# Optimization experiments

Measured on AMD Instinct MI355X. Metric: run time of the kernel, lower is better.

The kernel has to match this reference:

```python
import jax, jax.numpy as jnp
import numpy as np

N_NODES = 50000
N_ENT = 100000
N_REL = 200
DE = 100
DR = 100
B = 16
E2 = 600000
U = 500


def setup_inputs() -> dict:
    key = jax.random.key(0)
    ks = jax.random.split(key, 16)
    f32 = jnp.float32
    return {
        "entity_table": jax.random.normal(ks[0], (N_ENT, DE), f32),
        "relation_table": jax.random.normal(ks[1], (N_REL, DR), f32),
        "total_unseen_embedding": jax.random.normal(ks[2], (U, DE), f32),
        "att_mu": jax.random.normal(ks[3], (2 * N_REL, B), f32) * 0.1,
        "basis_mu": jax.random.normal(ks[4], (B, DE + DR, DE), f32) * 0.05,
        "root_mu": jax.random.normal(ks[5], (DE, DE), f32) * 0.1,
        "bias_mu": jnp.zeros((DE,), f32),
        "att_sigma": jax.random.normal(ks[6], (2 * N_REL, B), f32) * 0.1,
        "basis_sigma": jax.random.normal(ks[7], (B, DE + DR, DE), f32) * 0.05,
        "root_sigma": jax.random.normal(ks[8], (DE, DE), f32) * 0.1,
        "bias_sigma": jnp.zeros((DE,), f32),
        "node_id": jax.random.randint(ks[9], (N_NODES,), 0, N_ENT),
        "edge_index": jax.random.randint(ks[10], (2, E2), 0, N_NODES),
        "edge_type": jax.random.randint(ks[11], (E2,), 0, 2 * N_REL),
        "rel_index": jax.random.randint(ks[12], (E2,), 0, N_REL),
        "unseen_index": jax.random.randint(ks[13], (U,), 0, N_NODES),
    }


def gen_conv(m, edge_type, dst, x, att, basis, root, bias, n_nodes):
    """Basis-decomposed relational conv with mean aggregation (GENConv).

    m: [E, in] per-edge concat(x_src, rel_emb); msg_e = m_e @ (att[type_e] @ basis).
    Computed as sum_b coeff[:, b] * (m @ basis[b]) to avoid an [E, in, out] gather.
    """
    coeff = att[edge_type]  # [E, B]
    msg = coeff[:, 0:1] * (m @ basis[0])
    for b in range(1, basis.shape[0]):
        msg = msg + coeff[:, b:b + 1] * (m @ basis[b])
    agg = jax.ops.segment_sum(msg, dst, num_segments=n_nodes)  # [N, out]
    cnt = jax.ops.segment_sum(jnp.ones((m.shape[0],), m.dtype), dst,
                              num_segments=n_nodes)
    agg = agg / jnp.maximum(cnt, 1.0)[:, None]  # scatter-mean, empty nodes -> 0
    return agg + x @ root + bias


def reference(entity_table, relation_table, total_unseen_embedding,
              att_mu, basis_mu, root_mu, bias_mu,
              att_sigma, basis_sigma, root_sigma, bias_sigma,
              node_id, edge_index, edge_type, rel_index, unseen_index):
    x = entity_table[node_id]  # [N, De]
    x = x.at[unseen_index].set(total_unseen_embedding)
    rel_emb = relation_table[rel_index]  # [E, Dr]
    src, dst = edge_index[0], edge_index[1]
    m = jnp.concatenate([x[src], rel_emb], axis=1)  # [E, De+Dr]
    n = x.shape[0]
    mu = gen_conv(m, edge_type, dst, x, att_mu, basis_mu, root_mu, bias_mu, n)
    logvar = gen_conv(m, edge_type, dst, x, att_sigma, basis_sigma,
                      root_sigma, bias_sigma, n)
    # eval mode: reparameterize -> mu, dropout -> identity
    unseen = mu[unseen_index]
    return unseen, mu[unseen_index], logvar[unseen_index]
```

## Files before the change

kernel.cpp:

```cpp
#include <hip/hip_runtime.h>
#include <stdint.h>

#define E2V     600000
#define NNODES  50000
#define UCNT    500
#define DE      100
#define DOUT    100
#define NB      16
#define KTOT    3328
#define KCH     104
#define MROWS   512
#define HASHN   2048
#define HCAP    64
#define NREG    586
#define ECAP    96
#define TRB     832
#define OUTN    (3*UCNT*DOUT)

using short8 = __attribute__((ext_vector_type(8))) short;
using f32x4  = __attribute__((ext_vector_type(4))) float;

static constexpr size_t align256(size_t x){ return (x + 255) & ~size_t(255); }
static constexpr size_t OFF_HCNT = 0;
static constexpr size_t OFF_IHEA = align256(OFF_HCNT + NREG*4);
static constexpr size_t OFF_INEX = OFF_IHEA + MROWS*4;
static constexpr size_t OFF_HBUF = align256(OFF_INEX + MROWS*4);
static constexpr size_t OFF_GM   = align256(OFF_HBUF + (size_t)NREG*HCAP*4);
static constexpr size_t OFF_GS   = OFF_GM + (size_t)MROWS*KTOT*2;
static constexpr size_t OFF_BTM  = align256(OFF_GS + (size_t)MROWS*KTOT*2);
static constexpr size_t OFF_BTS  = OFF_BTM + (size_t)DOUT*KTOT*2;

__device__ __forceinline__ unsigned short f2b(float f){
    uint32_t u = __float_as_uint(f);
    uint32_t r = (u + 0x7FFFu + ((u >> 16) & 1u)) >> 16;
    return (unsigned short)r;
}

__device__ __forceinline__ uint32_t hh(int key){
    return (((uint32_t)key * 2654435761u) >> 16) & (HASHN - 1);
}
__device__ __forceinline__ void hins(int* hk, int* hv, int key, int val){
    uint32_t idx = hh(key);
    while (true){
        int k = hk[idx];
        if (k == key){ atomicMax(&hv[idx], val); return; }
        if (k == -1){
            int old = atomicCAS(&hk[idx], -1, key);
            if (old == -1 || old == key){ atomicMax(&hv[idx], val); return; }
        }
        idx = (idx + 1) & (HASHN - 1);
    }
}
__device__ __forceinline__ int hlook(const int* hk, const int* hv, int key){
    uint32_t idx = hh(key);
    while (true){
        int k = hk[idx];
        if (k == key) return hv[idx];
        if (k == -1)  return -1;
        idx = (idx + 1) & (HASHN - 1);
    }
}

__device__ __forceinline__ float bt_src(const float* __restrict__ basis,
                                        const float* __restrict__ root,
                                        const float* __restrict__ bias,
                                        int k, int j){
    if (j >= 100) return 0.f;
    if (k < 3200) return basis[k*100 + j];
    if (k < 3300) return root[(k-3200)*100 + j];
    if (k == 3300) return bias[j];
    return 0.f;
}

__global__ __launch_bounds__(256) void k1(
        const int* __restrict__ unseen_index, const int* __restrict__ eidx,
        int* __restrict__ hcnt, uint32_t* __restrict__ hbuf,
        int* __restrict__ ihead, int* __restrict__ inext,
        const float* __restrict__ bm, const float* __restrict__ bs,
        const float* __restrict__ rm, const float* __restrict__ rs,
        const float* __restrict__ qm, const float* __restrict__ qs,
        unsigned short* __restrict__ btm, unsigned short* __restrict__ bts){
    __shared__ int hk[HASHN], hv[HASHN];
    __shared__ float tile[32][33];
    __shared__ uint32_t sHit[HCAP];
    __shared__ int sN, sIH[MROWS];
    int bx = blockIdx.x, tid = threadIdx.x;

    if (bx < NREG){
        for (int i = tid; i < HASHN; i += 256){ hk[i] = -1; hv[i] = -1; }
        if (tid == 0) sN = 0;
        __syncthreads();
        for (int u = tid; u < UCNT; u += 256) hins(hk, hv, unseen_index[u], u);
        __syncthreads();
        int e0 = bx*1024 + tid*4;
        if (e0 < E2V){
            int4 d = *(const int4*)(eidx + E2V + e0);
            int s;
            s = hlook(hk, hv, d.x); if (s >= 0){ int p = atomicAdd(&sN,1); if (p < HCAP) sHit[p] = ((uint32_t)s<<21)|(uint32_t)(e0);   }
            s = hlook(hk, hv, d.y); if (s >= 0){ int p = atomicAdd(&sN,1); if (p < HCAP) sHit[p] = ((uint32_t)s<<21)|(uint32_t)(e0+1); }
            s = hlook(hk, hv, d.z); if (s >= 0){ int p = atomicAdd(&sN,1); if (p < HCAP) sHit[p] = ((uint32_t)s<<21)|(uint32_t)(e0+2); }
            s = hlook(hk, hv, d.w); if (s >= 0){ int p = atomicAdd(&sN,1); if (p < HCAP) sHit[p] = ((uint32_t)s<<21)|(uint32_t)(e0+3); }
        }
        __syncthreads();
        int n = sN < HCAP ? sN : HCAP;
        if (tid == 0) hcnt[bx] = n;
        if (tid < n) hbuf[bx*HCAP + tid] = sHit[tid];
        return;
    }
    if (bx < NREG + TRB){
        int b2 = bx - NREG;
        int kt = b2 % KCH, jt = (b2 / KCH) & 3, br = b2 / (KCH*4);
        const float* basis = br ? bs : bm;
        const float* root  = br ? rs : rm;
        const float* bias  = br ? qs : qm;
        unsigned short* bt = br ? bts : btm;
        int k0 = kt*32, j0 = jt*32;
        int tx = tid & 31, ty = tid >> 5;
        for (int r = ty; r < 32; r += 8)
            tile[r][tx] = bt_src(basis, root, bias, k0 + r, j0 + tx);
        __syncthreads();
        for (int r = ty; r < 32; r += 8){
            int j = j0 + r;
            if (j < 100) bt[(size_t)j*KTOT + k0 + tx] = f2b(tile[tx][r]);
        }
        return;
    }
    for (int i = tid; i < HASHN; i += 256){ hk[i] = -1; hv[i] = -1; }
    for (int i = tid; i < MROWS; i += 256) sIH[i] = -1;
    __syncthreads();
    for (int u = tid; u < UCNT; u += 256) hins(hk, hv, unseen_index[u], u);
    __syncthreads();
    for (int u = tid; u < UCNT; u += 256){
        int slot = hlook(hk, hv, unseen_index[u]);
        inext[u] = atomicExch(&sIH[slot], u);
    }
    __syncthreads();
    for (int i = tid; i < MROWS; i += 256) ihead[i] = sIH[i];
}

__global__ __launch_bounds__(256) void k_g(
        const int* __restrict__ hcnt, const uint32_t* __restrict__ hbuf,
        const int* __restrict__ unseen_index,
        const int* __restrict__ eidx,
        const int* __restrict__ etype, const int* __restrict__ rel_index,
        const int* __restrict__ node_id,
        const float* __restrict__ ent, const float* __restrict__ unseen,
        const float* __restrict__ rel,
        const float* __restrict__ am, const float* __restrict__ as_,
        unsigned short* __restrict__ Gm, unsigned short* __restrict__ Gs,
        float* __restrict__ out){
    int slot = blockIdx.x;
    int tid  = threadIdx.x;
    {
        int z0 = slot * 294;
        for (int i = z0 + tid; i < z0 + 294 && i < OUTN; i += 256) out[i] = 0.f;
    }
    __shared__ int hk[HASHN], hv[HASHN];
    __shared__ int sEdge[ECAP], sNE;
    __shared__ __align__(16) float sM[8][200];
    __shared__ __align__(16) float sAm[8][16], sAs[8][16];
    __shared__ const float* sPX[8];
    __shared__ const float* sPR[8];
    __shared__ int sT[8];

    for (int i = tid; i < HASHN; i += 256){ hk[i] = -1; hv[i] = -1; }
    if (tid == 0) sNE = 0;
    __syncthreads();
    for (int u = tid; u < UCNT; u += 256) hins(hk, hv, unseen_index[u], u);
    __syncthreads();
    for (int r = tid; r < NREG; r += 256){
        int c = hcnt[r];
        for (int i = 0; i < c; ++i){
            uint32_t h = hbuf[r*HCAP + i];
            if ((int)(h >> 21) == slot){
                int p = atomicAdd(&sNE, 1);
                if (p < ECAP) sEdge[p] = (int)(h & 0x1FFFFFu);
            }
        }
    }
    __syncthreads();
    int nT = sNE;
    int nE = nT > ECAP ? ECAP : nT;

    float gm[16], gs[16];
    #pragma unroll
    for (int b = 0; b < NB; ++b){ gm[b] = 0.f; gs[b] = 0.f; }

    for (int c0 = 0; c0 < nE; c0 += 8){
        int kc = nE - c0; if (kc > 8) kc = 8;
        if (tid < kc){
            int e = sEdge[c0 + tid];
            sT[tid] = etype[e];
            int s = eidx[e];
            int p = hlook(hk, hv, s);
            sPX[tid] = (p >= 0) ? unseen + (size_t)p*DE : ent + (size_t)node_id[s]*DE;
            sPR[tid] = rel + (size_t)rel_index[e]*DE;
        }
        __syncthreads();
        for (int q = tid; q < kc*50; q += 256){
            int eL = q / 50, s = q % 50;
            const float* base = (s < 25) ? sPX[eL] : sPR[eL];
            int off = (s < 25) ? s*4 : (s-25)*4;
            float4 v = *(const float4*)(base + off);
            int kb = (s < 25) ? s*4 : (s-25)*4 + 100;
            *(float4*)&sM[eL][kb] = v;
        }
        if (tid < kc*16){
            int eL = tid >> 4, b = tid & 15;
            int t = sT[eL];
            sAm[eL][b] = am[t*NB + b];
            sAs[eL][b] = as_[t*NB + b];
        }
        __syncthreads();
        if (tid < 200){
            for (int e = 0; e < kc; ++e){
                float mk = sM[e][tid];
                const float4* pa = (const float4*)&sAm[e][0];
                const float4* ps = (const float4*)&sAs[e][0];
                #pragma unroll
                for (int q = 0; q < 4; ++q){
                    float4 va = pa[q], vs = ps[q];
                    gm[q*4+0] += va.x*mk; gm[q*4+1] += va.y*mk;
                    gm[q*4+2] += va.z*mk; gm[q*4+3] += va.w*mk;
                    gs[q*4+0] += vs.x*mk; gs[q*4+1] += vs.y*mk;
                    gs[q*4+2] += vs.z*mk; gs[q*4+3] += vs.w*mk;
                }
            }
        }
        __syncthreads();
    }
    size_t row = (size_t)slot * KTOT;
    float inv = 1.f / fmaxf((float)nT, 1.f);
    if (tid < 200){
        #pragma unroll
        for (int b = 0; b < NB; ++b){
            Gm[row + b*200 + tid] = f2b(gm[b] * inv);
            Gs[row + b*200 + tid] = f2b(gs[b] * inv);
        }
    }
    if (tid < 100){
        float xv = (slot < UCNT) ? unseen[(size_t)slot*DE + tid] : 0.f;
        unsigned short h = f2b(xv);
        Gm[row + 3200 + tid] = h; Gs[row + 3200 + tid] = h;
    } else if (tid == 100){
        Gm[row + 3300] = f2b(1.f); Gs[row + 3300] = f2b(1.f);
    } else if (tid > 100 && tid < 128){
        Gm[row + 3200 + tid] = 0; Gs[row + 3200 + tid] = 0;
    }
}

__global__ __launch_bounds__(448) void k_gemm(
        const unsigned short* __restrict__ Gm, const unsigned short* __restrict__ Gs,
        const unsigned short* __restrict__ Btm, const unsigned short* __restrict__ Bts,
        const int* __restrict__ ihead, const int* __restrict__ inext,
        float* __restrict__ out){
    int bid = blockIdx.x;
    int br  = bid >> 7;
    int m32 = (bid >> 3) & 15;
    int ks  = bid & 7;
    int jt  = threadIdx.x >> 6;
    int lane = threadIdx.x & 63;
    const unsigned short* A  = br ? Gs : Gm;
    const unsigned short* Bt = br ? Bts : Btm;
    int rowa = lane & 15, ko = (lane >> 4) * 8;
    int j0 = (jt == 6) ? 84 : jt*16;
    int col = j0 + rowa;
    size_t kbase = (size_t)ks*416 + ko;
    const unsigned short* bp  = Bt + (size_t)col*KTOT + kbase;
    const unsigned short* ap0 = A  + (size_t)(m32*32 + rowa)*KTOT + kbase;
    const unsigned short* ap1 = ap0 + (size_t)16*KTOT;
    f32x4 acc0 = {0.f,0.f,0.f,0.f}, acc1 = {0.f,0.f,0.f,0.f};
    #pragma unroll
    for (int kc = 0; kc < 13; ++kc){
        short8 bv = *(const short8*)(bp + kc*32);
        acc0 = __builtin_amdgcn_mfma_f32_16x16x32_bf16(*(const short8*)(ap0 + kc*32), bv, acc0, 0, 0, 0);
        acc1 = __builtin_amdgcn_mfma_f32_16x16x32_bf16(*(const short8*)(ap1 + kc*32), bv, acc1, 0, 0, 0);
    }
    if (jt < 6 || col >= 96){
        #pragma unroll
        for (int mi = 0; mi < 2; ++mi){
            f32x4 acc = mi ? acc1 : acc0;
            int r0 = m32*32 + mi*16 + (lane >> 4)*4;
            #pragma unroll
            for (int r = 0; r < 4; ++r){
                int u = ihead[r0 + r];
                while (u >= 0){
                    if (br == 0){
                        atomicAdd(&out[(size_t)u*100 + col], acc[r]);
                        atomicAdd(&out[(size_t)(UCNT + u)*100 + col], acc[r]);
                    } else {
                        atomicAdd(&out[(size_t)(2*UCNT + u)*100 + col], acc[r]);
                    }
                    u = inext[u];
                }
            }
        }
    }
}

extern "C" void kernel_launch(void* const* d_in, const int* in_sizes, int n_in,
                              void* d_out, int out_size, void* d_ws, size_t ws_size,
                              hipStream_t stream){
    const float* ent        = (const float*)d_in[0];
    const float* rel_table  = (const float*)d_in[1];
    const float* unseen_emb = (const float*)d_in[2];
    const float* att_mu     = (const float*)d_in[3];
    const float* basis_mu   = (const float*)d_in[4];
    const float* root_mu    = (const float*)d_in[5];
    const float* bias_mu    = (const float*)d_in[6];
    const float* att_sig    = (const float*)d_in[7];
    const float* basis_sig  = (const float*)d_in[8];
    const float* root_sig   = (const float*)d_in[9];
    const float* bias_sig   = (const float*)d_in[10];
    const int* node_id      = (const int*)d_in[11];
    const int* edge_index   = (const int*)d_in[12];
    const int* edge_type    = (const int*)d_in[13];
    const int* rel_index    = (const int*)d_in[14];
    const int* unseen_index = (const int*)d_in[15];
    float* out = (float*)d_out;
    char* ws = (char*)d_ws;

    int* hcnt       = (int*)(ws + OFF_HCNT);
    int* ihead      = (int*)(ws + OFF_IHEA);
    int* inext      = (int*)(ws + OFF_INEX);
    uint32_t* hbuf  = (uint32_t*)(ws + OFF_HBUF);
    unsigned short* Gm  = (unsigned short*)(ws + OFF_GM);
    unsigned short* Gs  = (unsigned short*)(ws + OFF_GS);
    unsigned short* Btm = (unsigned short*)(ws + OFF_BTM);
    unsigned short* Bts = (unsigned short*)(ws + OFF_BTS);

    k1<<<NREG + TRB + 1, 256, 0, stream>>>(unseen_index, edge_index,
        hcnt, hbuf, ihead, inext,
        basis_mu, basis_sig, root_mu, root_sig, bias_mu, bias_sig, Btm, Bts);
    k_g<<<MROWS, 256, 0, stream>>>(hcnt, hbuf, unseen_index, edge_index, edge_type,
        rel_index, node_id, ent, unseen_emb, rel_table, att_mu, att_sig, Gm, Gs, out);
    k_gemm<<<256, 448, 0, stream>>>(Gm, Gs, Btm, Bts, ihead, inext, out);
}
```

Baseline: 53.21 us.

## Bucket edges per slot via global atomics and replace atomic output with split-K reduce kernel

The edge filter now uses fewer blocks, each scanning 8192 edges. Hits are appended directly into per-slot global edge lists with atomic counters, and each hit also stores a precomputed source slot. This removes the per-block hash rebuild and the full hit-buffer scan in k_g. The GEMM now uses 13 K-splits, writes partials to a buffer instead of atomically adding into the output, and a new k_out kernel sums the partials and scatters them to duplicate unseen indices. The cost is an extra memset and an extra kernel launch, plus global atomic contention on the slot counters.

```diff
diff --git a/kernel.cpp b/kernel.cpp
--- a/kernel.cpp
+++ b/kernel.cpp
@@ -8,27 +8,27 @@
 #define DOUT    100
 #define NB      16
 #define KTOT    3328
-#define KCH     104
 #define MROWS   512
 #define HASHN   2048
-#define HCAP    64
-#define NREG    586
-#define ECAP    96
+#define CAP     96
+#define NF      74
 #define TRB     832
-#define OUTN    (3*UCNT*DOUT)
+#define NKS     13
 
 using short8 = __attribute__((ext_vector_type(8))) short;
 using f32x4  = __attribute__((ext_vector_type(4))) float;
 
 static constexpr size_t align256(size_t x){ return (x + 255) & ~size_t(255); }
-static constexpr size_t OFF_HCNT = 0;
-static constexpr size_t OFF_IHEA = align256(OFF_HCNT + NREG*4);
+static constexpr size_t OFF_SCNT = 0;
+static constexpr size_t OFF_IHEA = align256(OFF_SCNT + MROWS*4);
 static constexpr size_t OFF_INEX = OFF_IHEA + MROWS*4;
-static constexpr size_t OFF_HBUF = align256(OFF_INEX + MROWS*4);
-static constexpr size_t OFF_GM   = align256(OFF_HBUF + (size_t)NREG*HCAP*4);
+static constexpr size_t OFF_ELIS = align256(OFF_INEX + MROWS*4);
+static constexpr size_t OFF_ESRC = align256(OFF_ELIS + (size_t)MROWS*CAP*4);
+static constexpr size_t OFF_GM   = align256(OFF_ESRC + (size_t)MROWS*CAP*2);
 static constexpr size_t OFF_GS   = OFF_GM + (size_t)MROWS*KTOT*2;
 static constexpr size_t OFF_BTM  = align256(OFF_GS + (size_t)MROWS*KTOT*2);
 static constexpr size_t OFF_BTS  = OFF_BTM + (size_t)DOUT*KTOT*2;
+static constexpr size_t OFF_P    = align256(OFF_BTS + (size_t)DOUT*KTOT*2);
 
 __device__ __forceinline__ unsigned short f2b(float f){
     uint32_t u = __float_as_uint(f);
@@ -74,7 +74,7 @@
 
 __global__ __launch_bounds__(256) void k1(
         const int* __restrict__ unseen_index, const int* __restrict__ eidx,
-        int* __restrict__ hcnt, uint32_t* __restrict__ hbuf,
+        int* __restrict__ scnt, int* __restrict__ elist, short* __restrict__ esrc,
         int* __restrict__ ihead, int* __restrict__ inext,
         const float* __restrict__ bm, const float* __restrict__ bs,
         const float* __restrict__ rm, const float* __restrict__ rs,
@@ -82,34 +82,38 @@
         unsigned short* __restrict__ btm, unsigned short* __restrict__ bts){
     __shared__ int hk[HASHN], hv[HASHN];
     __shared__ float tile[32][33];
-    __shared__ uint32_t sHit[HCAP];
-    __shared__ int sN, sIH[MROWS];
+    __shared__ int sIH[MROWS];
     int bx = blockIdx.x, tid = threadIdx.x;
 
-    if (bx < NREG){
+    if (bx < NF){
         for (int i = tid; i < HASHN; i += 256){ hk[i] = -1; hv[i] = -1; }
-        if (tid == 0) sN = 0;
         __syncthreads();
         for (int u = tid; u < UCNT; u += 256) hins(hk, hv, unseen_index[u], u);
         __syncthreads();
-        int e0 = bx*1024 + tid*4;
-        if (e0 < E2V){
+        for (int r = 0; r < 8; ++r){
+            int e0 = bx*8192 + (r*256 + tid)*4;
+            if (e0 >= E2V) break;
             int4 d = *(const int4*)(eidx + E2V + e0);
-            int s;
-            s = hlook(hk, hv, d.x); if (s >= 0){ int p = atomicAdd(&sN,1); if (p < HCAP) sHit[p] = ((uint32_t)s<<21)|(uint32_t)(e0);   }
-            s = hlook(hk, hv, d.y); if (s >= 0){ int p = atomicAdd(&sN,1); if (p < HCAP) sHit[p] = ((uint32_t)s<<21)|(uint32_t)(e0+1); }
-            s = hlook(hk, hv, d.z); if (s >= 0){ int p = atomicAdd(&sN,1); if (p < HCAP) sHit[p] = ((uint32_t)s<<21)|(uint32_t)(e0+2); }
-            s = hlook(hk, hv, d.w); if (s >= 0){ int p = atomicAdd(&sN,1); if (p < HCAP) sHit[p] = ((uint32_t)s<<21)|(uint32_t)(e0+3); }
-        }
-        __syncthreads();
-        int n = sN < HCAP ? sN : HCAP;
-        if (tid == 0) hcnt[bx] = n;
-        if (tid < n) hbuf[bx*HCAP + tid] = sHit[tid];
+            #pragma unroll
+            for (int j = 0; j < 4; ++j){
+                int dn = (j==0) ? d.x : (j==1) ? d.y : (j==2) ? d.z : d.w;
+                int s = hlook(hk, hv, dn);
+                if (s >= 0){
+                    int e = e0 + j;
+                    int srcp = hlook(hk, hv, eidx[e]);
+                    int pos = atomicAdd(&scnt[s], 1);
+                    if (pos < CAP){
+                        elist[s*CAP + pos] = e;
+                        esrc[s*CAP + pos] = (short)srcp;
+                    }
+                }
+            }
+        }
         return;
     }
-    if (bx < NREG + TRB){
-        int b2 = bx - NREG;
-        int kt = b2 % KCH, jt = (b2 / KCH) & 3, br = b2 / (KCH*4);
+    if (bx < NF + TRB){
+        int b2 = bx - NF;
+        int kt = b2 % 104, jt = (b2 / 104) & 3, br = b2 / 416;
         const float* basis = br ? bs : bm;
         const float* root  = br ? rs : rm;
         const float* bias  = br ? qs : qm;
@@ -139,49 +143,25 @@
 }
 
 __global__ __launch_bounds__(256) void k_g(
-        const int* __restrict__ hcnt, const uint32_t* __restrict__ hbuf,
-        const int* __restrict__ unseen_index,
+        const int* __restrict__ scnt, const int* __restrict__ elist,
+        const short* __restrict__ esrc,
         const int* __restrict__ eidx,
         const int* __restrict__ etype, const int* __restrict__ rel_index,
         const int* __restrict__ node_id,
         const float* __restrict__ ent, const float* __restrict__ unseen,
         const float* __restrict__ rel,
         const float* __restrict__ am, const float* __restrict__ as_,
-        unsigned short* __restrict__ Gm, unsigned short* __restrict__ Gs,
-        float* __restrict__ out){
+        unsigned short* __restrict__ Gm, unsigned short* __restrict__ Gs){
     int slot = blockIdx.x;
     int tid  = threadIdx.x;
-    {
-        int z0 = slot * 294;
-        for (int i = z0 + tid; i < z0 + 294 && i < OUTN; i += 256) out[i] = 0.f;
-    }
-    __shared__ int hk[HASHN], hv[HASHN];
-    __shared__ int sEdge[ECAP], sNE;
+    int nT = scnt[slot];
+    int nE = nT > CAP ? CAP : nT;
     __shared__ __align__(16) float sM[8][200];
     __shared__ __align__(16) float sAm[8][16], sAs[8][16];
     __shared__ const float* sPX[8];
     __shared__ const float* sPR[8];
     __shared__ int sT[8];
 
-    for (int i = tid; i < HASHN; i += 256){ hk[i] = -1; hv[i] = -1; }
-    if (tid == 0) sNE = 0;
-    __syncthreads();
-    for (int u = tid; u < UCNT; u += 256) hins(hk, hv, unseen_index[u], u);
-    __syncthreads();
-    for (int r = tid; r < NREG; r += 256){
-        int c = hcnt[r];
-        for (int i = 0; i < c; ++i){
-            uint32_t h = hbuf[r*HCAP + i];
-            if ((int)(h >> 21) == slot){
-                int p = atomicAdd(&sNE, 1);
-                if (p < ECAP) sEdge[p] = (int)(h & 0x1FFFFFu);
-            }
-        }
-    }
-    __syncthreads();
-    int nT = sNE;
-    int nE = nT > ECAP ? ECAP : nT;
-
     float gm[16], gs[16];
     #pragma unroll
     for (int b = 0; b < NB; ++b){ gm[b] = 0.f; gs[b] = 0.f; }
@@ -189,11 +169,11 @@
     for (int c0 = 0; c0 < nE; c0 += 8){
         int kc = nE - c0; if (kc > 8) kc = 8;
         if (tid < kc){
-            int e = sEdge[c0 + tid];
+            int e = elist[slot*CAP + c0 + tid];
             sT[tid] = etype[e];
-            int s = eidx[e];
-            int p = hlook(hk, hv, s);
-            sPX[tid] = (p >= 0) ? unseen + (size_t)p*DE : ent + (size_t)node_id[s]*DE;
+            int srcp = esrc[slot*CAP + c0 + tid];
+            sPX[tid] = (srcp >= 0) ? unseen + (size_t)srcp*DE
+                                   : ent + (size_t)node_id[eidx[e]]*DE;
             sPR[tid] = rel + (size_t)rel_index[e]*DE;
         }
         __syncthreads();
@@ -252,12 +232,12 @@
 __global__ __launch_bounds__(448) void k_gemm(
         const unsigned short* __restrict__ Gm, const unsigned short* __restrict__ Gs,
         const unsigned short* __restrict__ Btm, const unsigned short* __restrict__ Bts,
-        const int* __restrict__ ihead, const int* __restrict__ inext,
-        float* __restrict__ out){
+        float* __restrict__ P){
     int bid = blockIdx.x;
-    int br  = bid >> 7;
-    int m32 = (bid >> 3) & 15;
-    int ks  = bid & 7;
+    int br  = bid / 208;
+    int rem = bid % 208;
+    int m32 = rem & 15;
+    int ks  = rem >> 4;
     int jt  = threadIdx.x >> 6;
     int lane = threadIdx.x & 63;
     const unsigned short* A  = br ? Gs : Gm;
@@ -265,36 +245,49 @@
     int rowa = lane & 15, ko = (lane >> 4) * 8;
     int j0 = (jt == 6) ? 84 : jt*16;
     int col = j0 + rowa;
-    size_t kbase = (size_t)ks*416 + ko;
+    size_t kbase = (size_t)ks*256 + ko;
     const unsigned short* bp  = Bt + (size_t)col*KTOT + kbase;
     const unsigned short* ap0 = A  + (size_t)(m32*32 + rowa)*KTOT + kbase;
     const unsigned short* ap1 = ap0 + (size_t)16*KTOT;
     f32x4 acc0 = {0.f,0.f,0.f,0.f}, acc1 = {0.f,0.f,0.f,0.f};
     #pragma unroll
-    for (int kc = 0; kc < 13; ++kc){
+    for (int kc = 0; kc < 8; ++kc){
         short8 bv = *(const short8*)(bp + kc*32);
         acc0 = __builtin_amdgcn_mfma_f32_16x16x32_bf16(*(const short8*)(ap0 + kc*32), bv, acc0, 0, 0, 0);
         acc1 = __builtin_amdgcn_mfma_f32_16x16x32_bf16(*(const short8*)(ap1 + kc*32), bv, acc1, 0, 0, 0);
     }
     if (jt < 6 || col >= 96){
+        float* Pb = P + (size_t)(br*NKS + ks)*MROWS*100;
         #pragma unroll
         for (int mi = 0; mi < 2; ++mi){
             f32x4 acc = mi ? acc1 : acc0;
             int r0 = m32*32 + mi*16 + (lane >> 4)*4;
             #pragma unroll
-            for (int r = 0; r < 4; ++r){
-                int u = ihead[r0 + r];
-                while (u >= 0){
-                    if (br == 0){
-                        atomicAdd(&out[(size_t)u*100 + col], acc[r]);
-                        atomicAdd(&out[(size_t)(UCNT + u)*100 + col], acc[r]);
-                    } else {
-                        atomicAdd(&out[(size_t)(2*UCNT + u)*100 + col], acc[r]);
-                    }
-                    u = inext[u];
-                }
-            }
-        }
+            for (int r = 0; r < 4; ++r)
+                Pb[(size_t)(r0 + r)*100 + col] = acc[r];
+        }
+    }
+}
+
+__global__ __launch_bounds__(128) void k_out(
+        const float* __restrict__ P,
+        const int* __restrict__ ihead, const int* __restrict__ inext,
+        float* __restrict__ out){
+    int slot = blockIdx.x;
+    int tid  = threadIdx.x;
+    if (tid >= 100) return;
+    float mu = 0.f, sg = 0.f;
+    #pragma unroll
+    for (int ks = 0; ks < NKS; ++ks){
+        mu += P[((size_t)ks*MROWS + slot)*100 + tid];
+        sg += P[((size_t)(NKS + ks)*MROWS + slot)*100 + tid];
+    }
+    int u = ihead[slot];
+    while (u >= 0){
+        out[(size_t)u*100 + tid] = mu;
+        out[(size_t)(UCNT + u)*100 + tid] = mu;
+        out[(size_t)(2*UCNT + u)*100 + tid] = sg;
+        u = inext[u];
     }
 }
 
@@ -320,19 +313,23 @@
     float* out = (float*)d_out;
     char* ws = (char*)d_ws;
 
-    int* hcnt       = (int*)(ws + OFF_HCNT);
-    int* ihead      = (int*)(ws + OFF_IHEA);
-    int* inext      = (int*)(ws + OFF_INEX);
-    uint32_t* hbuf  = (uint32_t*)(ws + OFF_HBUF);
+    int* scnt   = (int*)(ws + OFF_SCNT);
+    int* ihead  = (int*)(ws + OFF_IHEA);
+    int* inext  = (int*)(ws + OFF_INEX);
+    int* elist  = (int*)(ws + OFF_ELIS);
+    short* esrc = (short*)(ws + OFF_ESRC);
     unsigned short* Gm  = (unsigned short*)(ws + OFF_GM);
     unsigned short* Gs  = (unsigned short*)(ws + OFF_GS);
     unsigned short* Btm = (unsigned short*)(ws + OFF_BTM);
     unsigned short* Bts = (unsigned short*)(ws + OFF_BTS);
-
-    k1<<<NREG + TRB + 1, 256, 0, stream>>>(unseen_index, edge_index,
-        hcnt, hbuf, ihead, inext,
+    float* P = (float*)(ws + OFF_P);
+
+    hipMemsetAsync(scnt, 0, MROWS*4, stream);
+    k1<<<NF + TRB + 1, 256, 0, stream>>>(unseen_index, edge_index,
+        scnt, elist, esrc, ihead, inext,
         basis_mu, basis_sig, root_mu, root_sig, bias_mu, bias_sig, Btm, Bts);
-    k_g<<<MROWS, 256, 0, stream>>>(hcnt, hbuf, unseen_index, edge_index, edge_type,
-        rel_index, node_id, ent, unseen_emb, rel_table, att_mu, att_sig, Gm, Gs, out);
-    k_gemm<<<256, 448, 0, stream>>>(Gm, Gs, Btm, Bts, ihead, inext, out);
-}
+    k_g<<<MROWS, 256, 0, stream>>>(scnt, elist, esrc, edge_index, edge_type,
+        rel_index, node_id, ent, unseen_emb, rel_table, att_mu, att_sig, Gm, Gs);
+    k_gemm<<<416, 448, 0, stream>>>(Gm, Gs, Btm, Bts, P);
+    k_out<<<MROWS, 128, 0, stream>>>(P, ihead, inext, out);
+}
```

After: 76.09 us. 1.43x slower.

## Replace atomic split-K accumulation with partial buffers and a reduction kernel

Applied to the files above, without the earlier changes.

The GEMM now splits K into 13 chunks of 256 instead of 8 chunks of 416, launching 416 blocks. Each block writes its partial tile to a workspace buffer rather than atomically adding into the output. A new k_out kernel sums the partials per row and scatters the results to every unseen index sharing that slot. This removes the output zeroing and the float atomics, and gives more GEMM parallelism. The cost is an extra kernel launch plus writing and re-reading about 2.6 MB of partials.

```diff
diff --git a/kernel.cpp b/kernel.cpp
--- a/kernel.cpp
+++ b/kernel.cpp
@@ -8,14 +8,13 @@
 #define DOUT    100
 #define NB      16
 #define KTOT    3328
-#define KCH     104
 #define MROWS   512
 #define HASHN   2048
 #define HCAP    64
 #define NREG    586
 #define ECAP    96
 #define TRB     832
-#define OUTN    (3*UCNT*DOUT)
+#define NKS     13
 
 using short8 = __attribute__((ext_vector_type(8))) short;
 using f32x4  = __attribute__((ext_vector_type(4))) float;
@@ -29,6 +28,7 @@
 static constexpr size_t OFF_GS   = OFF_GM + (size_t)MROWS*KTOT*2;
 static constexpr size_t OFF_BTM  = align256(OFF_GS + (size_t)MROWS*KTOT*2);
 static constexpr size_t OFF_BTS  = OFF_BTM + (size_t)DOUT*KTOT*2;
+static constexpr size_t OFF_P    = align256(OFF_BTS + (size_t)DOUT*KTOT*2);
 
 __device__ __forceinline__ unsigned short f2b(float f){
     uint32_t u = __float_as_uint(f);
@@ -109,7 +109,7 @@
     }
     if (bx < NREG + TRB){
         int b2 = bx - NREG;
-        int kt = b2 % KCH, jt = (b2 / KCH) & 3, br = b2 / (KCH*4);
+        int kt = b2 % 104, jt = (b2 / 104) & 3, br = b2 / 416;
         const float* basis = br ? bs : bm;
         const float* root  = br ? rs : rm;
         const float* bias  = br ? qs : qm;
@@ -147,14 +147,9 @@
         const float* __restrict__ ent, const float* __restrict__ unseen,
         const float* __restrict__ rel,
         const float* __restrict__ am, const float* __restrict__ as_,
-        unsigned short* __restrict__ Gm, unsigned short* __restrict__ Gs,
-        float* __restrict__ out){
+        unsigned short* __restrict__ Gm, unsigned short* __restrict__ Gs){
     int slot = blockIdx.x;
     int tid  = threadIdx.x;
-    {
-        int z0 = slot * 294;
-        for (int i = z0 + tid; i < z0 + 294 && i < OUTN; i += 256) out[i] = 0.f;
-    }
     __shared__ int hk[HASHN], hv[HASHN];
     __shared__ int sEdge[ECAP], sNE;
     __shared__ __align__(16) float sM[8][200];
@@ -252,12 +247,12 @@
 __global__ __launch_bounds__(448) void k_gemm(
         const unsigned short* __restrict__ Gm, const unsigned short* __restrict__ Gs,
         const unsigned short* __restrict__ Btm, const unsigned short* __restrict__ Bts,
-        const int* __restrict__ ihead, const int* __restrict__ inext,
-        float* __restrict__ out){
+        float* __restrict__ P){
     int bid = blockIdx.x;
-    int br  = bid >> 7;
-    int m32 = (bid >> 3) & 15;
-    int ks  = bid & 7;
+    int br  = bid / 208;
+    int rem = bid % 208;
+    int m32 = rem & 15;
+    int ks  = rem >> 4;
     int jt  = threadIdx.x >> 6;
     int lane = threadIdx.x & 63;
     const unsigned short* A  = br ? Gs : Gm;
@@ -265,36 +260,49 @@
     int rowa = lane & 15, ko = (lane >> 4) * 8;
     int j0 = (jt == 6) ? 84 : jt*16;
     int col = j0 + rowa;
-    size_t kbase = (size_t)ks*416 + ko;
+    size_t kbase = (size_t)ks*256 + ko;
     const unsigned short* bp  = Bt + (size_t)col*KTOT + kbase;
     const unsigned short* ap0 = A  + (size_t)(m32*32 + rowa)*KTOT + kbase;
     const unsigned short* ap1 = ap0 + (size_t)16*KTOT;
     f32x4 acc0 = {0.f,0.f,0.f,0.f}, acc1 = {0.f,0.f,0.f,0.f};
     #pragma unroll
-    for (int kc = 0; kc < 13; ++kc){
+    for (int kc = 0; kc < 8; ++kc){
         short8 bv = *(const short8*)(bp + kc*32);
         acc0 = __builtin_amdgcn_mfma_f32_16x16x32_bf16(*(const short8*)(ap0 + kc*32), bv, acc0, 0, 0, 0);
         acc1 = __builtin_amdgcn_mfma_f32_16x16x32_bf16(*(const short8*)(ap1 + kc*32), bv, acc1, 0, 0, 0);
     }
     if (jt < 6 || col >= 96){
+        float* Pb = P + (size_t)(br*NKS + ks)*MROWS*100;
         #pragma unroll
         for (int mi = 0; mi < 2; ++mi){
             f32x4 acc = mi ? acc1 : acc0;
             int r0 = m32*32 + mi*16 + (lane >> 4)*4;
             #pragma unroll
-            for (int r = 0; r < 4; ++r){
-                int u = ihead[r0 + r];
-                while (u >= 0){
-                    if (br == 0){
-                        atomicAdd(&out[(size_t)u*100 + col], acc[r]);
-                        atomicAdd(&out[(size_t)(UCNT + u)*100 + col], acc[r]);
-                    } else {
-                        atomicAdd(&out[(size_t)(2*UCNT + u)*100 + col], acc[r]);
-                    }
-                    u = inext[u];
-                }
-            }
-        }
+            for (int r = 0; r < 4; ++r)
+                Pb[(size_t)(r0 + r)*100 + col] = acc[r];
+        }
+    }
+}
+
+__global__ __launch_bounds__(128) void k_out(
+        const float* __restrict__ P,
+        const int* __restrict__ ihead, const int* __restrict__ inext,
+        float* __restrict__ out){
+    int slot = blockIdx.x;
+    int tid  = threadIdx.x;
+    if (tid >= 100) return;
+    float mu = 0.f, sg = 0.f;
+    #pragma unroll
+    for (int ks = 0; ks < NKS; ++ks){
+        mu += P[((size_t)ks*MROWS + slot)*100 + tid];
+        sg += P[((size_t)(NKS + ks)*MROWS + slot)*100 + tid];
+    }
+    int u = ihead[slot];
+    while (u >= 0){
+        out[(size_t)u*100 + tid] = mu;
+        out[(size_t)(UCNT + u)*100 + tid] = mu;
+        out[(size_t)(2*UCNT + u)*100 + tid] = sg;
+        u = inext[u];
     }
 }
 
@@ -328,11 +336,13 @@
     unsigned short* Gs  = (unsigned short*)(ws + OFF_GS);
     unsigned short* Btm = (unsigned short*)(ws + OFF_BTM);
     unsigned short* Bts = (unsigned short*)(ws + OFF_BTS);
+    float* P = (float*)(ws + OFF_P);
 
     k1<<<NREG + TRB + 1, 256, 0, stream>>>(unseen_index, edge_index,
         hcnt, hbuf, ihead, inext,
         basis_mu, basis_sig, root_mu, root_sig, bias_mu, bias_sig, Btm, Bts);
     k_g<<<MROWS, 256, 0, stream>>>(hcnt, hbuf, unseen_index, edge_index, edge_type,
-        rel_index, node_id, ent, unseen_emb, rel_table, att_mu, att_sig, Gm, Gs, out);
-    k_gemm<<<256, 448, 0, stream>>>(Gm, Gs, Btm, Bts, ihead, inext, out);
-}
+        rel_index, node_id, ent, unseen_emb, rel_table, att_mu, att_sig, Gm, Gs);
+    k_gemm<<<416, 448, 0, stream>>>(Gm, Gs, Btm, Bts, P);
+    k_out<<<MROWS, 128, 0, stream>>>(P, ihead, inext, out);
+}
```

New measurement: 52.14 us. 2.0% less time.
